# Kernel tuning notes

Measured on AMD Instinct MI355X. Metric: run time of the kernel, lower is better.

Reference implementation:

```python
import jax, jax.numpy as jnp
import numpy as np

C = 1024
H = 16
EPS = 1e-5


def setup_inputs() -> dict:
    key = jax.random.key(0)
    ks = jax.random.split(key, 10)
    B, S = 2, 2048
    s = 1.0 / np.sqrt(C)
    return {
        "hidden_states": jax.random.normal(ks[0], (B, C, S), dtype=jnp.float32),
        "attention_mask": jnp.ones((B, S), dtype=jnp.int32),
        "gn_weight": jnp.ones((C,), dtype=jnp.float32),
        "gn_bias": jnp.zeros((C,), dtype=jnp.float32),
        "Wq": jax.random.normal(ks[1], (C, C), dtype=jnp.float32) * s,
        "bq": jnp.zeros((C,), dtype=jnp.float32),
        "Wk": jax.random.normal(ks[2], (C, C), dtype=jnp.float32) * s,
        "bk": jnp.zeros((C,), dtype=jnp.float32),
        "Wv": jax.random.normal(ks[3], (C, C), dtype=jnp.float32) * s,
        "bv": jnp.zeros((C,), dtype=jnp.float32),
        "Wo": jax.random.normal(ks[4], (C, C), dtype=jnp.float32) * s,
        "bo": jnp.zeros((C,), dtype=jnp.float32),
    }


def reference(hidden_states, attention_mask, gn_weight, gn_bias,
              Wq, bq, Wk, bk, Wv, bv, Wo, bo):
    # hidden_states: (B, C, S); attention_mask: (B, S)
    B, Cc, S = hidden_states.shape
    D = Cc // H
    residual = hidden_states

    # GroupNorm with 1 group: normalize over (C, S) per sample
    mean = jnp.mean(hidden_states, axis=(1, 2), keepdims=True)
    var = jnp.var(hidden_states, axis=(1, 2), keepdims=True)
    x = (hidden_states - mean) * jax.lax.rsqrt(var + EPS)
    x = x * gn_weight[None, :, None] + gn_bias[None, :, None]

    x = jnp.transpose(x, (0, 2, 1))  # (B, S, C)
    q = x @ Wq.T + bq
    k = x @ Wk.T + bk
    v = x @ Wv.T + bv

    # (B, H, S, D)
    q = q.reshape(B, S, H, D).transpose(0, 2, 1, 3)
    k = k.reshape(B, S, H, D).transpose(0, 2, 1, 3)
    v = v.reshape(B, S, H, D).transpose(0, 2, 1, 3)

    scale = 1.0 / np.sqrt(np.sqrt(D))
    scores = jnp.einsum('bhqd,bhkd->bhqk', q * scale, k * scale)
    mask = attention_mask[:, None, None, :]  # (B,1,1,S) broadcast over heads/query
    scores = jnp.where(mask == 0, -jnp.inf, scores)
    probs = jax.nn.softmax(scores, axis=-1)

    out = jnp.einsum('bhqk,bhkd->bhqd', probs, v)  # (B,H,S,D)
    out = out.transpose(0, 2, 1, 3).reshape(B, S, Cc)
    out = out @ Wo.T + bo
    out = jnp.transpose(out, (0, 2, 1))  # (B, C, S)
    return out + residual
```

## Files before the change

### kernel.cpp

```cpp
#include <hip/hip_runtime.h>
#include <hip/hip_bf16.h>

#define B_ 2
#define C_ 1024
#define S_ 2048
#define H_ 16
#define KDIM 1024

typedef __attribute__((ext_vector_type(8))) short short8_t;
typedef __attribute__((ext_vector_type(4))) float f32x4;
typedef __attribute__((ext_vector_type(16))) float f32x16;
typedef __attribute__((ext_vector_type(4))) int i32x4;

__device__ __forceinline__ void glds16(const void* g, void* l) {
  __builtin_amdgcn_global_load_lds((const __attribute__((address_space(1))) void*)g,
                                   (__attribute__((address_space(3))) void*)l, 16, 0, 0);
}

__device__ __forceinline__ unsigned short f2bf(float f) {
  __hip_bfloat16 h = __float2bfloat16(f);
  return __builtin_bit_cast(unsigned short, h);
}

__device__ __forceinline__ unsigned pkbf(float lo, float hi) {
  unsigned r;
  asm("v_cvt_pk_bf16_f32 %0, %1, %2" : "=v"(r) : "v"(lo), "v"(hi));
  return r;
}

__device__ __forceinline__ void plswap(unsigned &a, unsigned &b) {
  asm("v_permlane32_swap_b32 %0, %1" : "+v"(a), "+v"(b));
}

__device__ __forceinline__ float max3f(float a, float b, float c) {
  float r;
  asm("v_max3_f32 %0, %1, %2, %3" : "=v"(r) : "v"(a), "v"(b), "v"(c));
  return r;
}

__device__ __forceinline__ float max16v(const f32x16& v) {
  float a = max3f(v[0], v[1], v[2]);
  float b = max3f(v[3], v[4], v[5]);
  float c = max3f(v[6], v[7], v[8]);
  float d = max3f(v[9], v[10], v[11]);
  float e = max3f(v[12], v[13], v[14]);
  float f = max3f(a, b, v[15]);
  float g = max3f(c, d, e);
  return fmaxf(f, g);
}

__global__ __launch_bounds__(256) void cvt_w4(const float* __restrict__ a,
                                              const float* __restrict__ b,
                                              const float* __restrict__ c,
                                              const float* __restrict__ d,
                                              unsigned short* __restrict__ o) {
  int g = blockIdx.x >> 10;
  const float* src = (g == 0) ? a : (g == 1) ? b : (g == 2) ? c : d;
  int i = (blockIdx.x & 1023) * 256 + threadIdx.x;
  float4 v = ((const float4*)src)[i];
  short4 r;
  r.x = (short)f2bf(v.x); r.y = (short)f2bf(v.y);
  r.z = (short)f2bf(v.z); r.w = (short)f2bf(v.w);
  ((short4*)(o))[(size_t)g * 262144 + i] = r;
}

__global__ __launch_bounds__(256) void stats1(const float* __restrict__ x,
                                              float2* __restrict__ part) {
  int bid = blockIdx.x;
  int b = bid >> 8, chunk = bid & 255;
  const float4* p = (const float4*)(x + (size_t)b*(C_*S_) + (size_t)chunk*8192);
  int t = threadIdx.x;
  float s = 0.f, q = 0.f;
#pragma unroll
  for (int i = 0; i < 8; ++i) {
    float4 v = p[t + i*256];
    s += v.x + v.y + v.z + v.w;
    q += v.x*v.x + v.y*v.y + v.z*v.z + v.w*v.w;
  }
#pragma unroll
  for (int d = 1; d < 64; d <<= 1) { s += __shfl_xor(s, d); q += __shfl_xor(q, d); }
  __shared__ float2 wsum[4];
  if ((t & 63) == 0) wsum[t >> 6] = make_float2(s, q);
  __syncthreads();
  if (t == 0) {
    float S = 0.f, Q = 0.f;
    for (int i = 0; i < 4; ++i) { S += wsum[i].x; Q += wsum[i].y; }
    part[bid] = make_float2(S, Q);
  }
}

__global__ __launch_bounds__(256) void stats2(const float2* __restrict__ part,
                                              float* __restrict__ stats) {
  int b = blockIdx.x;
  int t = threadIdx.x;
  float2 v = part[b*256 + t];
  float s = v.x, q = v.y;
#pragma unroll
  for (int d = 1; d < 64; d <<= 1) { s += __shfl_xor(s, d); q += __shfl_xor(q, d); }
  __shared__ float2 wsum[4];
  if ((t & 63) == 0) wsum[t >> 6] = make_float2(s, q);
  __syncthreads();
  if (t == 0) {
    float S = 0.f, Q = 0.f;
    for (int i = 0; i < 4; ++i) { S += wsum[i].x; Q += wsum[i].y; }
    const float invN = 1.0f / (float)(C_*S_);
    float mean = S * invN;
    float var = Q * invN - mean*mean;
    stats[b*2]   = mean;
    stats[b*2+1] = rsqrtf(var + 1e-5f);
  }
}

__global__ __launch_bounds__(256) void normt(const float* __restrict__ x,
                                             const float* __restrict__ gw,
                                             const float* __restrict__ gb,
                                             const float* __restrict__ stats,
                                             unsigned short* __restrict__ xt) {
  __shared__ short lds[64*72];
  int bid = blockIdx.x;
  int b = bid >> 9, rem = bid & 511;
  int ct = rem >> 5, st = rem & 31;
  float mean = stats[b*2], rstd = stats[b*2+1];
  int t = threadIdx.x;
  int r = t >> 2, seg = t & 3;
  int c = ct*64 + r;
  float wsc = gw[c] * rstd;
  float bof = gb[c] - mean * wsc;
  const float4* src = (const float4*)(x + (size_t)b*(C_*S_) + (size_t)c*S_ + st*64 + seg*16);
#pragma unroll
  for (int j = 0; j < 4; ++j) {
    float4 v = src[j];
    int sl = seg*16 + j*4;
    lds[(sl+0)*72 + r] = (short)f2bf(v.x*wsc + bof);
    lds[(sl+1)*72 + r] = (short)f2bf(v.y*wsc + bof);
    lds[(sl+2)*72 + r] = (short)f2bf(v.z*wsc + bof);
    lds[(sl+3)*72 + r] = (short)f2bf(v.w*wsc + bof);
  }
  __syncthreads();
  int sl = t >> 2;
  __attribute__((aligned(16))) unsigned short tmp[16];
#pragma unroll
  for (int j = 0; j < 16; ++j) tmp[j] = (unsigned short)lds[sl*72 + seg*16 + j];
  unsigned short* dst = xt + ((size_t)b*S_ + st*64 + sl) * C_ + ct*64 + seg*16;
  *(short8_t*)dst       = *(const short8_t*)tmp;
  *(short8_t*)(dst + 8) = *(const short8_t*)(tmp + 8);
}

__global__ __launch_bounds__(256)
void gemm_qk(const unsigned short* __restrict__ A,
             const unsigned short* __restrict__ Bm,
             const float* __restrict__ bq,
             const float* __restrict__ bk,
             unsigned short* __restrict__ outp) {
  __shared__ __attribute__((aligned(16))) short As[128*64];
  __shared__ __attribute__((aligned(16))) short Bs[128*64];
  int bid = blockIdx.x;
  int sbid = (bid & 7) * 64 + (bid >> 3);
  int bm = sbid >> 4, bn = sbid & 15;
  int m0 = bm << 7, n0 = bn << 7;
  int t = threadIdx.x, l = t & 63, wid = t >> 6;
  int wr = wid >> 1, wc = wid & 1;

  int rsb = wid*8 + (l >> 3);
  int slot_src = (l & 7) ^ (l >> 3);
  const unsigned short* a_src = A + (size_t)(m0 + rsb) * KDIM + slot_src * 8;
  const unsigned short* b_src = Bm + (size_t)(n0 + rsb) * KDIM + slot_src * 8;
  char* adst = (char*)As + wid*1024;
  char* bdst = (char*)Bs + wid*1024;

  f32x4 acc[4][4] = {};

  for (int kt = 0; kt < KDIM; kt += 64) {
    __syncthreads();
#pragma unroll
    for (int i = 0; i < 4; ++i) {
      glds16(a_src + (size_t)(i*32)*KDIM + kt, adst + i*4096);
      glds16(b_src + (size_t)(i*32)*KDIM + kt, bdst + i*4096);
    }
    __syncthreads();
#pragma unroll
    for (int kk = 0; kk < 2; ++kk) {
      short8_t af[4], bf[4];
#pragma unroll
      for (int mi = 0; mi < 4; ++mi) {
        int row = wr*64 + mi*16 + (l & 15);
        int slot = (kk*4 + (l >> 4)) ^ (row & 7);
        af[mi] = *(const short8_t*)((const char*)As + row*128 + slot*16);
      }
#pragma unroll
      for (int ni = 0; ni < 4; ++ni) {
        int row = wc*64 + ni*16 + (l & 15);
        int slot = (kk*4 + (l >> 4)) ^ (row & 7);
        bf[ni] = *(const short8_t*)((const char*)Bs + row*128 + slot*16);
      }
#pragma unroll
      for (int mi = 0; mi < 4; ++mi)
#pragma unroll
        for (int ni = 0; ni < 4; ++ni)
          acc[mi][ni] = __builtin_amdgcn_mfma_f32_16x16x32_bf16(af[mi], bf[ni], acc[mi][ni], 0, 0, 0);
    }
  }

  int gcol0 = n0 + wc*64;
  const float* bp = (gcol0 & 1024) ? bk : bq;
  unsigned short* ob = outp + ((gcol0 & 1024) ? 4194304u : 0u);
  int hd0 = gcol0 & 1023;
#pragma unroll
  for (int mi = 0; mi < 4; ++mi)
#pragma unroll
    for (int ni = 0; ni < 4; ++ni)
#pragma unroll
      for (int r = 0; r < 4; ++r) {
        int gm = m0 + wr*64 + mi*16 + ((l >> 4) << 2) + r;
        int hd = hd0 + ni*16 + (l & 15);
        float v = acc[mi][ni][r] + bp[hd];
        size_t off = ((size_t)((gm >> 11)*H_ + (hd >> 6)) * S_ + (gm & 2047)) * 64 + (hd & 63);
        ob[off] = f2bf(v);
      }
}

template<int EPI>
__global__ __launch_bounds__(256)
void gemm_nt(const unsigned short* __restrict__ A,
             const unsigned short* __restrict__ Bm,
             const float* __restrict__ bias,
             const float* __restrict__ resid,
             void* __restrict__ outp,
             int nbn) {
  __shared__ __attribute__((aligned(16))) short As[64*64];
  __shared__ __attribute__((aligned(16))) short Bs[128*64];
  int nwg = gridDim.x;
  int bid = blockIdx.x;
  int cpx = nwg >> 3;
  int sbid = (bid & 7) * cpx + (bid >> 3);
  int bm = sbid / nbn, bn = sbid % nbn;
  int m0 = bm << 6, n0 = bn << 7;
  int t = threadIdx.x;
  int l = t & 63, wid = t >> 6;

  int r_st = t >> 3;
  int slot_src = (t & 7) ^ (r_st & 7);
  const unsigned short* a_src = A + (size_t)(m0 + r_st) * KDIM + slot_src * 8;
  const unsigned short* b_src = Bm + (size_t)(n0 + r_st) * KDIM + slot_src * 8;
  char* As_base = (char*)As + wid*1024;
  char* Bs_base = (char*)Bs + wid*1024;

  f32x4 acc[4][2] = {};

  for (int kt = 0; kt < KDIM; kt += 64) {
    __syncthreads();
    glds16(a_src + kt, As_base);
    glds16(a_src + (size_t)32*KDIM + kt, As_base + 4096);
#pragma unroll
    for (int i = 0; i < 4; ++i)
      glds16(b_src + (size_t)(i*32)*KDIM + kt, Bs_base + i*4096);
    __syncthreads();
#pragma unroll
    for (int kk = 0; kk < 2; ++kk) {
      short8_t af[4], bfr[2];
#pragma unroll
      for (int mi = 0; mi < 4; ++mi) {
        int row = mi*16 + (l & 15);
        int slot = (kk*4 + (l >> 4)) ^ (row & 7);
        af[mi] = *(const short8_t*)((const char*)As + row*128 + slot*16);
      }
#pragma unroll
      for (int ni = 0; ni < 2; ++ni) {
        int row = wid*32 + ni*16 + (l & 15);
        int slot = (kk*4 + (l >> 4)) ^ (row & 7);
        bfr[ni] = *(const short8_t*)((const char*)Bs + row*128 + slot*16);
      }
#pragma unroll
      for (int mi = 0; mi < 4; ++mi)
#pragma unroll
        for (int ni = 0; ni < 2; ++ni)
          acc[mi][ni] = __builtin_amdgcn_mfma_f32_16x16x32_bf16(af[mi], bfr[ni], acc[mi][ni], 0, 0, 0);
    }
  }

#pragma unroll
  for (int mi = 0; mi < 4; ++mi) {
#pragma unroll
    for (int ni = 0; ni < 2; ++ni) {
#pragma unroll
      for (int r = 0; r < 4; ++r) {
        int gm = m0 + mi*16 + ((l >> 4) << 2) + r;
        int gn = n0 + wid*32 + ni*16 + (l & 15);
        float v = acc[mi][ni][r];
        v += bias[gm];
        size_t off = (size_t)(gn >> 11) * ((size_t)C_*S_) + (size_t)gm * S_ + (gn & 2047);
        if (EPI == 1) {
          ((unsigned short*)outp)[off] = f2bf(v);
        } else {
          ((float*)outp)[off] = v + resid[off];
        }
      }
    }
  }
}

__global__ __launch_bounds__(512, 4)
void attn_kernel(const unsigned short* __restrict__ Q,
                 const unsigned short* __restrict__ Kt,
                 const unsigned short* __restrict__ Vt,
                 const int* __restrict__ mask,
                 unsigned short* __restrict__ outp) {
  __shared__ __attribute__((aligned(16))) char lds[65536];
  __shared__ __attribute__((aligned(8)))  unsigned char maskb[256];
  __shared__ int tflag[32];

  int bid = blockIdx.x;
  int bid2 = (bid & 7) * 64 + (bid >> 3);
  int bh = bid2 >> 4, qt = bid2 & 15;
  int b = bh >> 4, h = bh & 15;
  int t = threadIdx.x, l = t & 63, wid = t >> 6;
  int quad = wid >> 2, qw = wid & 3;
  int hh = l >> 5;

  if (t < 256) {
    const i32x4* mp = (const i32x4*)(mask + b * S_) + t * 2;
    i32x4 m0 = mp[0], m1 = mp[1];
    unsigned by = (unsigned)(m0[0]!=0) | ((unsigned)(m0[1]!=0)<<1) | ((unsigned)(m0[2]!=0)<<2) | ((unsigned)(m0[3]!=0)<<3)
                | ((unsigned)(m1[0]!=0)<<4) | ((unsigned)(m1[1]!=0)<<5) | ((unsigned)(m1[2]!=0)<<6) | ((unsigned)(m1[3]!=0)<<7);
    maskb[t] = (unsigned char)by;
  }
  __syncthreads();
  if (t < 32) {
    unsigned long long v = ((const unsigned long long*)maskb)[t];
    tflag[t] = (v == 0xFFFFFFFFFFFFFFFFull) ? 1 : 0;
  }

  int q0 = qt*128 + qw*32;
  const unsigned short* qp = Q + ((size_t)bh * S_ + q0 + (l & 31)) * 64 + hh * 8;
  short8_t qf[4];
#pragma unroll
  for (int c = 0; c < 4; ++c) qf[c] = *(const short8_t*)(qp + c*16);

  int kbase = quad << 10;
  int row_st = qw*16 + (l >> 3);
  int slot_st = (l & 7) ^ (l >> 3);
  const unsigned short* kp = Kt + ((size_t)bh * S_ + kbase + row_st) * 64 + slot_st * 8;
  const unsigned short* vp = Vt + ((size_t)bh * 64 + row_st) * S_ + kbase + slot_st * 8;
  char* kdst = lds + quad*16384 + qw*2048;
  char* vdst = kdst + 32768;

  unsigned ko[8];
#pragma unroll
  for (int c = 0; c < 4; ++c) {
    unsigned slot = (unsigned)((c*2 + hh) ^ (l & 7)) * 16u;
    ko[c]   = (unsigned)(quad*16384) + (unsigned)(l & 31)*128u + slot;
    ko[c+4] = ko[c] + 4096u;
  }

  const short8_t vones = {0x3F80, 0x3F80, 0x3F80, 0x3F80, 0x3F80, 0x3F80, 0x3F80, 0x3F80};
  const float SC = 0.18033688011112042f;
  float m_run = 0.f, msc = 0.f;
  f32x16 oc0 = {}, oc1 = {}, lsum = {};

  glds16(kp,                kdst);
  glds16(kp + 8*64,         kdst + 1024);
  glds16(vp,                vdst);
  glds16(vp + (size_t)8*S_, vdst + 1024);
  const unsigned short* kn = kp + 64*64;
  const unsigned short* vn = vp + 64;
  int lt = 0;

#define ATILE(BUF)                                                              \
  do {                                                                          \
    __syncthreads();                                                            \
    glds16(kn,                kdst + ((BUF)^1)*8192);                           \
    glds16(kn + 8*64,         kdst + ((BUF)^1)*8192 + 1024);                    \
    glds16(vn,                vdst + ((BUF)^1)*8192);                           \
    glds16(vn + (size_t)8*S_, vdst + ((BUF)^1)*8192 + 1024);                    \
    kn += 4096; vn += 64;                                                       \
    f32x16 st0 = {}, st1 = {};                                                  \
    __builtin_amdgcn_s_setprio(1);                                              \
    _Pragma("unroll")                                                           \
    for (int c = 0; c < 4; ++c) {                                               \
      short8_t kf0 = *(const short8_t*)(lds + ko[c]   + (BUF)*8192);            \
      short8_t kf1 = *(const short8_t*)(lds + ko[c+4] + (BUF)*8192);            \
      st0 = __builtin_amdgcn_mfma_f32_32x32x16_bf16(kf0, qf[c], st0, 0, 0, 0);  \
      st1 = __builtin_amdgcn_mfma_f32_32x32x16_bf16(kf1, qf[c], st1, 0, 0, 0);  \
    }                                                                           \
    __builtin_amdgcn_s_setprio(0);                                              \
    _Pragma("unroll")                                                           \
    for (int r = 0; r < 16; ++r) {                                              \
      st0[r] = __builtin_amdgcn_exp2f(fmaf(st0[r], SC, -msc));                  \
      st1[r] = __builtin_amdgcn_exp2f(fmaf(st1[r], SC, -msc));                  \
    }                                                                           \
    if (!tflag[(kbase >> 6) + lt]) {                                            \
      _Pragma("unroll")                                                         \
      for (int r = 0; r < 16; ++r) {                                            \
        int kl = kbase + lt*64 + (r & 3) + 8*(r >> 2) + 4*hh;                   \
        if (!((maskb[kl >> 3] >> (kl & 7)) & 1)) st0[r] = 0.f;                  \
        kl += 32;                                                               \
        if (!((maskb[kl >> 3] >> (kl & 7)) & 1)) st1[r] = 0.f;                  \
      }                                                                         \
    }                                                                           \
    float pmax = fmaxf(max16v(st0), max16v(st1));                               \
    short8_t pa[4];                                                             \
    {                                                                           \
      unsigned a0 = pkbf(st0[0],  st0[1]),  b0 = pkbf(st0[4],  st0[5]);         \
      unsigned a1 = pkbf(st0[2],  st0[3]),  b1 = pkbf(st0[6],  st0[7]);         \
      plswap(a0, b0); plswap(a1, b1);                                           \
      i32x4 w0 = {(int)a0, (int)a1, (int)b0, (int)b1};                          \
      pa[0] = __builtin_bit_cast(short8_t, w0);                                 \
      unsigned a2 = pkbf(st0[8],  st0[9]),  b2 = pkbf(st0[12], st0[13]);        \
      unsigned a3 = pkbf(st0[10], st0[11]), b3 = pkbf(st0[14], st0[15]);        \
      plswap(a2, b2); plswap(a3, b3);                                           \
      i32x4 w1 = {(int)a2, (int)a3, (int)b2, (int)b3};                          \
      pa[1] = __builtin_bit_cast(short8_t, w1);                                 \
      unsigned a4 = pkbf(st1[0],  st1[1]),  b4 = pkbf(st1[4],  st1[5]);         \
      unsigned a5 = pkbf(st1[2],  st1[3]),  b5 = pkbf(st1[6],  st1[7]);         \
      plswap(a4, b4); plswap(a5, b5);                                           \
      i32x4 w2 = {(int)a4, (int)a5, (int)b4, (int)b5};                          \
      pa[2] = __builtin_bit_cast(short8_t, w2);                                 \
      unsigned a6 = pkbf(st1[8],  st1[9]),  b6 = pkbf(st1[12], st1[13]);        \
      unsigned a7 = pkbf(st1[10], st1[11]), b7 = pkbf(st1[14], st1[15]);        \
      plswap(a6, b6); plswap(a7, b7);                                           \
      i32x4 w3 = {(int)a6, (int)a7, (int)b6, (int)b7};                          \
      pa[3] = __builtin_bit_cast(short8_t, w3);                                 \
    }                                                                           \
    __builtin_amdgcn_s_setprio(1);                                              \
    _Pragma("unroll")                                                           \
    for (int kc = 0; kc < 4; ++kc) {                                            \
      short8_t vf0 = *(const short8_t*)(lds + ko[kc]   + 32768 + (BUF)*8192);   \
      short8_t vf1 = *(const short8_t*)(lds + ko[kc+4] + 32768 + (BUF)*8192);   \
      oc0 = __builtin_amdgcn_mfma_f32_32x32x16_bf16(vf0, pa[kc], oc0, 0, 0, 0); \
      oc1 = __builtin_amdgcn_mfma_f32_32x32x16_bf16(vf1, pa[kc], oc1, 0, 0, 0); \
      lsum = __builtin_amdgcn_mfma_f32_32x32x16_bf16(vones, pa[kc], lsum, 0, 0, 0); \
    }                                                                           \
    __builtin_amdgcn_s_setprio(0);                                              \
    if (__any(pmax > 148.0f)) {                                                 \
      float pm = fmaxf(pmax, __shfl_xor(pmax, 32));                             \
      float smax = (__log2f(pm) + msc) / SC;                                    \
      float nm = fmaxf(m_run, smax);                                            \
      float fac = __builtin_amdgcn_exp2f((m_run - nm) * SC);                    \
      _Pragma("unroll")                                                         \
      for (int r = 0; r < 16; ++r) { oc0[r] *= fac; oc1[r] *= fac; lsum[r] *= fac; } \
      m_run = nm; msc = nm * SC;                                                \
    }                                                                           \
    ++lt;                                                                       \
  } while (0)

  for (int tp = 0; tp < 8; ++tp) {
    ATILE(0);
    ATILE(1);
  }
#undef ATILE

  __syncthreads();
  if (quad == 1) {
    char* obuf = lds + qw*8192 + l*128;
#pragma unroll
    for (int j = 0; j < 4; ++j) {
      f32x4 u0 = { oc0[4*j], oc0[4*j+1], oc0[4*j+2], oc0[4*j+3] };
      *(f32x4*)(obuf + ((j ^ (l & 7)) * 16)) = u0;
      f32x4 u1 = { oc1[4*j], oc1[4*j+1], oc1[4*j+2], oc1[4*j+3] };
      *(f32x4*)(obuf + (((j+4) ^ (l & 7)) * 16)) = u1;
    }
    *(float2*)(lds + 32768 + (qw*64 + l)*8) = make_float2(lsum[0], m_run);
  }
  __syncthreads();
  if (quad == 0) {
    float2 lm1 = *(const float2*)(lds + 32768 + (qw*64 + l)*8);
    float M  = fmaxf(m_run, lm1.y);
    float a0 = __builtin_amdgcn_exp2f((m_run - M) * SC);
    float a1 = __builtin_amdgcn_exp2f((lm1.y - M) * SC);
    float lc = lsum[0] * a0 + lm1.x * a1;
    float inv = 1.f / lc;
    float s0 = a0 * inv, s1 = a1 * inv;
    const char* obuf = lds + qw*8192 + l*128;
#pragma unroll
    for (int j = 0; j < 4; ++j) {
      f32x4 u0 = *(const f32x4*)(obuf + ((j ^ (l & 7)) * 16));
      oc0[4*j]   = oc0[4*j]  *s0 + u0[0]*s1;
      oc0[4*j+1] = oc0[4*j+1]*s0 + u0[1]*s1;
      oc0[4*j+2] = oc0[4*j+2]*s0 + u0[2]*s1;
      oc0[4*j+3] = oc0[4*j+3]*s0 + u0[3]*s1;
      f32x4 u1 = *(const f32x4*)(obuf + (((j+4) ^ (l & 7)) * 16));
      oc1[4*j]   = oc1[4*j]  *s0 + u1[0]*s1;
      oc1[4*j+1] = oc1[4*j+1]*s0 + u1[1]*s1;
      oc1[4*j+2] = oc1[4*j+2]*s0 + u1[2]*s1;
      oc1[4*j+3] = oc1[4*j+3]*s0 + u1[3]*s1;
    }

    unsigned short* obase = outp + ((size_t)b * S_ + q0 + (l & 31)) * C_ + h*64 + hh*8;
#pragma unroll
    for (int dt = 0; dt < 2; ++dt) {
      const f32x16& oc = dt ? oc1 : oc0;
      unsigned a0w = pkbf(oc[0],  oc[1]),  b0w = pkbf(oc[4],  oc[5]);
      unsigned a1w = pkbf(oc[2],  oc[3]),  b1w = pkbf(oc[6],  oc[7]);
      plswap(a0w, b0w); plswap(a1w, b1w);
      i32x4 w0 = {(int)a0w, (int)a1w, (int)b0w, (int)b1w};
      *(i32x4*)(obase + dt*32) = w0;
      unsigned a2w = pkbf(oc[8],  oc[9]),  b2w = pkbf(oc[12], oc[13]);
      unsigned a3w = pkbf(oc[10], oc[11]), b3w = pkbf(oc[14], oc[15]);
      plswap(a2w, b2w); plswap(a3w, b3w);
      i32x4 w1 = {(int)a2w, (int)a3w, (int)b2w, (int)b3w};
      *(i32x4*)(obase + dt*32 + 16) = w1;
    }
  }
}

extern "C" void kernel_launch(void* const* d_in, const int* in_sizes, int n_in,
                              void* d_out, int out_size, void* d_ws, size_t ws_size,
                              hipStream_t stream) {
  const float* hs = (const float*)d_in[0];
  const int*   msk = (const int*)d_in[1];
  const float* gw = (const float*)d_in[2];
  const float* gb = (const float*)d_in[3];
  const float* Wq = (const float*)d_in[4];
  const float* bq = (const float*)d_in[5];
  const float* Wk = (const float*)d_in[6];
  const float* bk = (const float*)d_in[7];
  const float* Wv = (const float*)d_in[8];
  const float* bv = (const float*)d_in[9];
  const float* Wo = (const float*)d_in[10];
  const float* bo = (const float*)d_in[11];

  char* ws = (char*)d_ws;
  float*  stats = (float*)(ws);
  float2* part  = (float2*)(ws + 256);
  unsigned short* wq_b = (unsigned short*)(ws + 8192);
  unsigned short* wk_b = wq_b + 1048576;
  unsigned short* wv_b = wk_b + 1048576;
  unsigned short* wo_b = wv_b + 1048576;
  unsigned short* x_b  = wo_b + 1048576;
  unsigned short* q_b  = x_b  + 4194304;
  unsigned short* k_b  = q_b  + 4194304;
  unsigned short* vt_b = k_b  + 4194304;
  unsigned short* ao_b = vt_b + 4194304;

  cvt_w4<<<4096, 256, 0, stream>>>(Wq, Wk, Wv, Wo, wq_b);

  stats1<<<512, 256, 0, stream>>>(hs, part);
  stats2<<<2, 256, 0, stream>>>(part, stats);
  normt<<<1024, 256, 0, stream>>>(hs, gw, gb, stats, x_b);

  gemm_qk<<<512, 256, 0, stream>>>(x_b, wq_b, bq, bk, q_b);
  gemm_nt<1><<<512, 256, 0, stream>>>(wv_b, x_b, bv, nullptr, vt_b, 32);

  attn_kernel<<<512, 512, 0, stream>>>(q_b, k_b, vt_b, msk, ao_b);

  gemm_nt<2><<<512, 256, 0, stream>>>(wo_b, ao_b, bo, hs, d_out, 32);
}
```

Before: 124.1 us.

## Fuse V projection into QK GEMM and fold stats reduction into normalize

Removes the separate stats2 kernel by having every normt block redundantly reduce the 256 partial sums itself. Merges the V projection into the Q/K GEMM as one 768-block launch over a 3072-wide concatenated weight, with V tiles transposed through shared memory before being stored as V^T. This saves two launches and improves occupancy of the projection GEMM. In exchange, each normt block repeats the partial-sum reduction, and V now uses 128x128 tiles with an extra LDS transpose pass.

After: 126.9 us. 1.02x slower.

```diff
diff --git a/kernel.cpp b/kernel.cpp
--- a/kernel.cpp
+++ b/kernel.cpp
@@ -89,39 +89,31 @@
   }
 }
 
-__global__ __launch_bounds__(256) void stats2(const float2* __restrict__ part,
-                                              float* __restrict__ stats) {
-  int b = blockIdx.x;
-  int t = threadIdx.x;
-  float2 v = part[b*256 + t];
-  float s = v.x, q = v.y;
-#pragma unroll
-  for (int d = 1; d < 64; d <<= 1) { s += __shfl_xor(s, d); q += __shfl_xor(q, d); }
-  __shared__ float2 wsum[4];
-  if ((t & 63) == 0) wsum[t >> 6] = make_float2(s, q);
-  __syncthreads();
-  if (t == 0) {
-    float S = 0.f, Q = 0.f;
-    for (int i = 0; i < 4; ++i) { S += wsum[i].x; Q += wsum[i].y; }
-    const float invN = 1.0f / (float)(C_*S_);
-    float mean = S * invN;
-    float var = Q * invN - mean*mean;
-    stats[b*2]   = mean;
-    stats[b*2+1] = rsqrtf(var + 1e-5f);
-  }
-}
-
 __global__ __launch_bounds__(256) void normt(const float* __restrict__ x,
                                              const float* __restrict__ gw,
                                              const float* __restrict__ gb,
-                                             const float* __restrict__ stats,
+                                             const float2* __restrict__ part,
                                              unsigned short* __restrict__ xt) {
   __shared__ short lds[64*72];
+  __shared__ float2 wsum2[4];
   int bid = blockIdx.x;
   int b = bid >> 9, rem = bid & 511;
   int ct = rem >> 5, st = rem & 31;
-  float mean = stats[b*2], rstd = stats[b*2+1];
   int t = threadIdx.x;
+
+  float2 pv = part[b*256 + t];
+  float s = pv.x, q = pv.y;
+#pragma unroll
+  for (int d = 1; d < 64; d <<= 1) { s += __shfl_xor(s, d); q += __shfl_xor(q, d); }
+  if ((t & 63) == 0) wsum2[t >> 6] = make_float2(s, q);
+  __syncthreads();
+  float S = 0.f, Q = 0.f;
+#pragma unroll
+  for (int i = 0; i < 4; ++i) { S += wsum2[i].x; Q += wsum2[i].y; }
+  const float invN = 1.0f / (float)(C_*S_);
+  float mean = S * invN;
+  float rstd = rsqrtf(Q * invN - mean*mean + 1e-5f);
+
   int r = t >> 2, seg = t & 3;
   int c = ct*64 + r;
   float wsc = gw[c] * rstd;
@@ -147,16 +139,19 @@
 }
 
 __global__ __launch_bounds__(256)
-void gemm_qk(const unsigned short* __restrict__ A,
-             const unsigned short* __restrict__ Bm,
-             const float* __restrict__ bq,
-             const float* __restrict__ bk,
-             unsigned short* __restrict__ outp) {
-  __shared__ __attribute__((aligned(16))) short As[128*64];
-  __shared__ __attribute__((aligned(16))) short Bs[128*64];
+void gemm_qkv(const unsigned short* __restrict__ A,
+              const unsigned short* __restrict__ Bm,
+              const float* __restrict__ bq,
+              const float* __restrict__ bk,
+              const float* __restrict__ bv,
+              unsigned short* __restrict__ outqk,
+              unsigned short* __restrict__ outv) {
+  __shared__ __attribute__((aligned(16))) short smem[128*128];
+  short* As = smem;
+  short* Bs = smem + 8192;
   int bid = blockIdx.x;
-  int sbid = (bid & 7) * 64 + (bid >> 3);
-  int bm = sbid >> 4, bn = sbid & 15;
+  int sbid = (bid & 7) * 96 + (bid >> 3);
+  int bm = sbid / 24, bn = sbid % 24;
   int m0 = bm << 7, n0 = bn << 7;
   int t = threadIdx.x, l = t & 63, wid = t >> 6;
   int wr = wid >> 1, wc = wid & 1;
@@ -201,22 +196,47 @@
     }
   }
 
-  int gcol0 = n0 + wc*64;
-  const float* bp = (gcol0 & 1024) ? bk : bq;
-  unsigned short* ob = outp + ((gcol0 & 1024) ? 4194304u : 0u);
-  int hd0 = gcol0 & 1023;
-#pragma unroll
-  for (int mi = 0; mi < 4; ++mi)
-#pragma unroll
-    for (int ni = 0; ni < 4; ++ni)
-#pragma unroll
-      for (int r = 0; r < 4; ++r) {
-        int gm = m0 + wr*64 + mi*16 + ((l >> 4) << 2) + r;
-        int hd = hd0 + ni*16 + (l & 15);
-        float v = acc[mi][ni][r] + bp[hd];
-        size_t off = ((size_t)((gm >> 11)*H_ + (hd >> 6)) * S_ + (gm & 2047)) * 64 + (hd & 63);
-        ob[off] = f2bf(v);
-      }
+  if (bn < 16) {
+    int gcol0 = n0 + wc*64;
+    const float* bp = (gcol0 & 1024) ? bk : bq;
+    unsigned short* ob = outqk + ((gcol0 & 1024) ? 4194304u : 0u);
+    int hd0 = gcol0 & 1023;
+#pragma unroll
+    for (int mi = 0; mi < 4; ++mi)
+#pragma unroll
+      for (int ni = 0; ni < 4; ++ni)
+#pragma unroll
+        for (int r = 0; r < 4; ++r) {
+          int gm = m0 + wr*64 + mi*16 + ((l >> 4) << 2) + r;
+          int hd = hd0 + ni*16 + (l & 15);
+          float v = acc[mi][ni][r] + bp[hd];
+          size_t off = ((size_t)((gm >> 11)*H_ + (hd >> 6)) * S_ + (gm & 2047)) * 64 + (hd & 63);
+          ob[off] = f2bf(v);
+        }
+  } else {
+    int hdbase = n0 - 2048;
+    __syncthreads();
+#pragma unroll
+    for (int ni = 0; ni < 4; ++ni) {
+      int cl = wc*64 + ni*16 + (l & 15);
+      float bvv = bv[hdbase + cl];
+#pragma unroll
+      for (int mi = 0; mi < 4; ++mi)
+#pragma unroll
+        for (int r = 0; r < 4; ++r) {
+          int rl = wr*64 + mi*16 + ((l >> 4) << 2) + r;
+          smem[cl*128 + rl] = (short)f2bf(acc[mi][ni][r] + bvv);
+        }
+    }
+    __syncthreads();
+    int b = m0 >> 11, s0 = m0 & 2047;
+    int rn = t >> 1, seg = (t & 1) << 6;
+    const char* srcp = (const char*)smem + rn*256 + seg*2;
+    unsigned short* dstp = outv + ((size_t)(b*1024 + hdbase + rn)) * 2048 + s0 + seg;
+#pragma unroll
+    for (int j = 0; j < 8; ++j)
+      *(i32x4*)(dstp + j*8) = *(const i32x4*)(srcp + j*16);
+  }
 }
 
 template<int EPI>
@@ -520,7 +540,6 @@
   const float* bo = (const float*)d_in[11];
 
   char* ws = (char*)d_ws;
-  float*  stats = (float*)(ws);
   float2* part  = (float2*)(ws + 256);
   unsigned short* wq_b = (unsigned short*)(ws + 8192);
   unsigned short* wk_b = wq_b + 1048576;
@@ -535,11 +554,9 @@
   cvt_w4<<<4096, 256, 0, stream>>>(Wq, Wk, Wv, Wo, wq_b);
 
   stats1<<<512, 256, 0, stream>>>(hs, part);
-  stats2<<<2, 256, 0, stream>>>(part, stats);
-  normt<<<1024, 256, 0, stream>>>(hs, gw, gb, stats, x_b);
-
-  gemm_qk<<<512, 256, 0, stream>>>(x_b, wq_b, bq, bk, q_b);
-  gemm_nt<1><<<512, 256, 0, stream>>>(wv_b, x_b, bv, nullptr, vt_b, 32);
+  normt<<<1024, 256, 0, stream>>>(hs, gw, gb, part, x_b);
+
+  gemm_qkv<<<768, 256, 0, stream>>>(x_b, wq_b, bq, bk, bv, q_b, vt_b);
 
   attn_kernel<<<512, 512, 0, stream>>>(q_b, k_b, vt_b, msk, ao_b);
 
```
